# Performance work log

Hardware: AMD Instinct MI355X
Metric: run time of the kernel (lower is better)

## Reference

```python
import jax, jax.numpy as jnp
import numpy as np

# Dimensions (match init_kwargs)
N, B = 32, 16384            # num_elements (agents), batch_size
SD, AD, AD2 = 128, 64, 64   # state_dim, action_dim, action_dim2
IDIM = SD + AD              # per-agent encoder input (obs + act)
H, HEADS = 256, 4           # hidden_dim, attend_heads
AT = H // HEADS             # attend_dim = 64
ODIM = AD                   # critic output = action_dim


def setup_inputs() -> dict:
    key = jax.random.key(0)
    ks = jax.random.split(key, 20)
    g = lambda k, shape: (jax.random.normal(k, shape, jnp.float32) * 0.05)
    return {
        "agent_inputs": jax.random.normal(ks[0], (N, B, IDIM), jnp.float32),
        "state_agent": jax.random.normal(ks[1], (B, SD), jnp.float32),
        "meanfield": jax.random.normal(ks[2], (B, AD), jnp.float32),
        "meanfield2": jax.random.normal(ks[3], (B, AD2), jnp.float32),
        # per-agent critic encoders (enc_fc1)
        "enc_W": g(ks[4], (N, IDIM, H)), "enc_b": g(ks[5], (N, H)),
        # state / meanfield / meanfield2 encoders
        "sW": g(ks[6], (SD, H)), "sb": g(ks[7], (H,)),
        "mfW": g(ks[8], (AD, H)), "mfb": g(ks[9], (H,)),
        "mf2W": g(ks[10], (AD2, H)), "mf2b": g(ks[11], (H,)),
        # per-head key / selector (bias-free) and value extractors
        "Wk": g(ks[12], (HEADS, H, AT)),
        "Wsel": g(ks[13], (HEADS, H, AT)),
        "Wv": g(ks[14], (HEADS, H, AT)), "bv": g(ks[15], (HEADS, AT)),
        # critic head: Linear(4H->H) + LeakyReLU + Linear(H->odim)
        "W1": g(ks[16], (4 * H, H)), "b1": g(ks[17], (H,)),
        "W2": g(ks[18], (H, ODIM)), "b2": g(ks[19], (ODIM,)),
    }


def reference(agent_inputs, state_agent, meanfield, meanfield2,
              enc_W, enc_b, sW, sb, mfW, mfb, mf2W, mf2b,
              Wk, Wsel, Wv, bv, W1, b1, W2, b2):
    lrelu = jax.nn.leaky_relu  # default negative_slope=0.01, matches nn.LeakyReLU
    # Per-agent (obs,act) encoders: [N,B,H]
    sa = lrelu(jnp.einsum('nbi,nih->nbh', agent_inputs, enc_W) + enc_b[:, None, :])
    s_enc = lrelu(state_agent @ sW + sb)          # [B,H]
    mf_enc = lrelu(meanfield @ mfW + mfb)         # [B,H]
    mf2_enc = lrelu(meanfield2 @ mf2W + mf2b)     # [B,H]
    # agents = [0]; keys/values come from all agents except agent 0
    others = sa[1:]                               # [N-1,B,H]
    keys = jnp.einsum('nbh,ehd->enbd', others, Wk)                       # [E,N-1,B,AT]
    vals = lrelu(jnp.einsum('nbh,ehd->enbd', others, Wv) + bv[:, None, None, :])
    sel = jnp.einsum('bh,ehd->ebd', s_enc, Wsel)                         # [E,B,AT]
    logits = jnp.einsum('ebd,enbd->ebn', sel, keys) / jnp.sqrt(jnp.float32(AT))
    w = jax.nn.softmax(logits, axis=-1)                                  # over N-1 agents
    other_vals = jnp.einsum('ebn,enbd->ebd', w, vals)                    # [E,B,AT]
    # concatenate heads in order, matching torch cat over per-head results
    other_flat = jnp.transpose(other_vals, (1, 0, 2)).reshape(B, HEADS * AT)
    critic_in = jnp.concatenate([s_enc, mf_enc, mf2_enc, other_flat], axis=1)  # [B,4H]
    h1 = lrelu(critic_in @ W1 + b1)
    return h1 @ W2 + b2                                                  # all_q: [B,ODIM]
```

## Files before the change

### kernel.cpp

```cpp
#include <hip/hip_runtime.h>
#include <hip/hip_bf16.h>

#define N_AG   32
#define B_SZ   16384
#define SD_    128
#define AD_    64
#define IDIM_  192
#define H_     256
#define HEADS_ 4
#define AT_    64
#define NO_    31

typedef __attribute__((ext_vector_type(8))) short bf16x8_t;
typedef __attribute__((ext_vector_type(4))) float f32x4_t;
typedef __attribute__((ext_vector_type(4))) unsigned int u32x4_t;

__device__ inline unsigned short f2bfu(float f){
  union { __hip_bfloat16 h; unsigned short u; } cv;
  cv.h = __float2bfloat16(f);
  return cv.u;
}
__device__ inline float bflo(unsigned int u){
  union { float f; unsigned int i; } c; c.i = u << 16; return c.f;
}
__device__ inline float bfhi(unsigned int u){
  union { float f; unsigned int i; } c; c.i = u & 0xffff0000u; return c.f;
}

__device__ inline void gll16(const unsigned short* g, unsigned short* l) {
  __builtin_amdgcn_global_load_lds(
      (const __attribute__((address_space(1))) unsigned int*)g,
      (__attribute__((address_space(3))) unsigned int*)l, 16, 0, 0);
}

__device__ inline float dot8(bf16x8_t a, bf16x8_t b, float acc){
  u32x4_t au = __builtin_bit_cast(u32x4_t, a);
  u32x4_t bu = __builtin_bit_cast(u32x4_t, b);
  #pragma unroll
  for (int i = 0; i < 4; i++) {
    acc = fmaf(bflo(au[i]), bflo(bu[i]), acc);
    acc = fmaf(bfhi(au[i]), bfhi(bu[i]), acc);
  }
  return acc;
}

__global__ __launch_bounds__(256) void k_prep(
    const float* __restrict__ encW, const float* __restrict__ sW,
    const float* __restrict__ mfW,  const float* __restrict__ mf2W,
    const float* __restrict__ W1,   const float* __restrict__ W2,
    const float* __restrict__ Wv,   const float* __restrict__ Wsel,
    const float* __restrict__ Wk,
    unsigned short* __restrict__ encWt, unsigned short* __restrict__ sWt,
    unsigned short* __restrict__ mfWt,  unsigned short* __restrict__ mf2Wt,
    unsigned short* __restrict__ W1t,   unsigned short* __restrict__ W2t,
    unsigned short* __restrict__ WvT,   unsigned short* __restrict__ Mct)
{
  const int bid = blockIdx.x, tid = threadIdx.x;
  auto tr = [&](const float* src, unsigned short* dst, int K, int N, int idx){
    int kn = K * N;
    int b = idx / kn, i = idx - b * kn;
    int n = i / K, k = i - n * K;
    dst[(long)b * kn + i] = f2bfu(src[(long)b * kn + (long)k * N + n]);
  };
  if (bid < 5952)        tr(encW + 192*256, encWt, 192, 256, bid*256 + tid);
  else if (bid < 6080)   tr(sW,   sWt,  128, 256, (bid-5952)*256 + tid);
  else if (bid < 6144)   tr(mfW,  mfWt,  64, 256, (bid-6080)*256 + tid);
  else if (bid < 6208)   tr(mf2W, mf2Wt, 64, 256, (bid-6144)*256 + tid);
  else if (bid < 7232)   tr(W1,   W1t, 1024, 256, (bid-6208)*256 + tid);
  else if (bid < 7296)   tr(W2,   W2t,  256,  64, (bid-7232)*256 + tid);
  else if (bid < 7552)   tr(Wv,   WvT,  256,  64, (bid-7296)*256 + tid);
  else {
    int idx = (bid - 7552) * 256 + tid;
    int hp = idx & 255, eh = idx >> 8;
    int e = eh >> 8, h = eh & 255;
    const float* ws = Wsel + ((long)e * 256 + hp) * 64;
    const float* wk = Wk   + ((long)e * 256 + h ) * 64;
    float s = 0.f;
    #pragma unroll 8
    for (int d = 0; d < 64; d++) s += ws[d] * wk[d];
    Mct[idx] = f2bfu(0.125f * s);
  }
}

template<bool AF32, bool LRELU, bool OUTF32>
__global__ __launch_bounds__(512, 2) void k_gemm2(
    const void* __restrict__ Ap, int lda, long strideA,
    const unsigned short* __restrict__ Bt, long strideB,
    const float* __restrict__ bias, long strideBias,
    void* __restrict__ Cp, int ldc, long strideC,
    int K)
{
  __shared__ __align__(16) unsigned short Alds[2][64 * 64];
  __shared__ __align__(16) unsigned short Blds[2][256 * 64];

  const int tid = threadIdx.x;
  const int lane = tid & 63, w = tid >> 6;
  const int wr = w >> 2, wc = w & 3;
  const int lr = lane & 15, lg = lane >> 4;
  const int bm = blockIdx.x, bn = blockIdx.y, bz = blockIdx.z;

  f32x4_t acc[2][4];
  #pragma unroll
  for (int i = 0; i < 2; i++)
    #pragma unroll
    for (int j = 0; j < 4; j++) acc[i][j] = (f32x4_t){0.f, 0.f, 0.f, 0.f};

  const unsigned short* Bb = Bt + bz * strideB + (long)(bn * 256) * K;
  const float* Af32 = AF32 ? (const float*)Ap + bz * strideA + (long)(bm * 64) * lda : nullptr;
  const unsigned short* Abf = AF32 ? nullptr
      : (const unsigned short*)Ap + bz * strideA + (long)(bm * 64) * lda;
  const int nt = K >> 6;

  float4 ar0, ar1;

  auto stageB = [&](int buf, int k0){
    #pragma unroll
    for (int i = 0; i < 4; i++) {
      int c = i * 512 + tid;
      int n = c >> 3, sl = c & 7;
      gll16(Bb + (long)n * K + k0 + (((sl ^ (n & 7)) & 7) << 3), &Blds[buf][c * 8]);
    }
  };
  auto issueA = [&](int buf, int k0){
    if (AF32) {
      int r0 = tid >> 4, q0 = tid & 15;
      ar0 = *reinterpret_cast<const float4*>(Af32 + (long)r0 * lda + k0 + q0 * 4);
      int c1 = tid + 512, r1 = c1 >> 4, q1 = c1 & 15;
      ar1 = *reinterpret_cast<const float4*>(Af32 + (long)r1 * lda + k0 + q1 * 4);
    } else {
      int row = tid >> 3, sl = tid & 7;
      gll16(Abf + (long)row * lda + k0 + (((sl ^ (row & 7)) & 7) << 3),
            &Alds[buf][tid * 8]);
    }
  };
  auto writeA = [&](int buf){
    if (AF32) {
      {
        int c = tid, row = c >> 4, q = c & 15;
        ushort4 u;
        u.x = f2bfu(ar0.x); u.y = f2bfu(ar0.y); u.z = f2bfu(ar0.z); u.w = f2bfu(ar0.w);
        int di = row * 64 + ((((q >> 1) ^ (row & 7)) & 7) << 3) + ((q & 1) << 2);
        *reinterpret_cast<ushort4*>(&Alds[buf][di]) = u;
      }
      {
        int c = tid + 512, row = c >> 4, q = c & 15;
        ushort4 u;
        u.x = f2bfu(ar1.x); u.y = f2bfu(ar1.y); u.z = f2bfu(ar1.z); u.w = f2bfu(ar1.w);
        int di = row * 64 + ((((q >> 1) ^ (row & 7)) & 7) << 3) + ((q & 1) << 2);
        *reinterpret_cast<ushort4*>(&Alds[buf][di]) = u;
      }
    }
  };

  issueA(0, 0);
  stageB(0, 0);
  writeA(0);
  __builtin_amdgcn_sched_barrier(0);
  if (nt > 1) { issueA(1, 64); stageB(1, 64); }
  __builtin_amdgcn_sched_barrier(0);

  for (int t = 0; t < nt; t++) {
    const int cur = t & 1;
    if (t + 1 < nt) {
      if (AF32) asm volatile("s_waitcnt vmcnt(6) lgkmcnt(0)" ::: "memory");
      else      asm volatile("s_waitcnt vmcnt(5) lgkmcnt(0)" ::: "memory");
    } else {
      asm volatile("s_waitcnt vmcnt(0) lgkmcnt(0)" ::: "memory");
    }
    __builtin_amdgcn_s_barrier();
    __builtin_amdgcn_sched_barrier(0);

    bf16x8_t af[2][2], bf[4][2];
    #pragma unroll
    for (int mf = 0; mf < 2; mf++)
      #pragma unroll
      for (int kk = 0; kk < 2; kk++) {
        int row = wr * 32 + mf * 16 + lr;
        af[mf][kk] = *reinterpret_cast<const bf16x8_t*>(
            &Alds[cur][row * 64 + ((((kk * 4 + lg) ^ (row & 7)) & 7) << 3)]);
      }
    #pragma unroll
    for (int nf = 0; nf < 4; nf++)
      #pragma unroll
      for (int kk = 0; kk < 2; kk++) {
        int n = wc * 64 + nf * 16 + lr;
        bf[nf][kk] = *reinterpret_cast<const bf16x8_t*>(
            &Blds[cur][n * 64 + ((((kk * 4 + lg) ^ (n & 7)) & 7) << 3)]);
      }
    #pragma unroll
    for (int kk = 0; kk < 2; kk++)
      #pragma unroll
      for (int mf = 0; mf < 2; mf++)
        #pragma unroll
        for (int nf = 0; nf < 4; nf++)
          acc[mf][nf] = __builtin_amdgcn_mfma_f32_16x16x32_bf16(af[mf][kk], bf[nf][kk], acc[mf][nf], 0, 0, 0);

    __builtin_amdgcn_sched_barrier(0);
    if (t + 1 < nt) writeA(cur ^ 1);
    if (t + 2 < nt) {
      __builtin_amdgcn_s_barrier();
      __builtin_amdgcn_sched_barrier(0);
      issueA(cur, (t + 2) * 64);
      stageB(cur, (t + 2) * 64);
      __builtin_amdgcn_sched_barrier(0);
    }
  }

  const float* bp = bias ? bias + bz * strideBias : nullptr;
  #pragma unroll
  for (int nf = 0; nf < 4; nf++) {
    int col = bn * 256 + wc * 64 + nf * 16 + lr;
    float bvv = bp ? bp[col] : 0.f;
    #pragma unroll
    for (int mf = 0; mf < 2; mf++) {
      #pragma unroll
      for (int r = 0; r < 4; r++) {
        int row = bm * 64 + wr * 32 + mf * 16 + lg * 4 + r;
        float v = acc[mf][nf][r] + bvv;
        if (LRELU) v = v > 0.f ? v : 0.01f * v;
        if (OUTF32)
          ((float*)Cp)[bz * strideC + (long)row * ldc + col] = v;
        else
          ((unsigned short*)Cp)[bz * strideC + (long)row * ldc + col] = f2bfu(v);
      }
    }
  }
}

__global__ __launch_bounds__(512) void k_attnw(
    const unsigned short* __restrict__ others,
    const unsigned short* __restrict__ qbuf,
    float* __restrict__ wbuf,
    float* __restrict__ wsum)
{
  __shared__ __align__(16) unsigned short olds[2][16 * 256];

  const int tid = threadIdx.x;
  const int bm = blockIdx.x;
  const int row = tid >> 5, sub = tid & 31;
  const int e = sub >> 3, ch = sub & 7;
  const long grow = (long)bm * 16 + row;

  bf16x8_t qr[4];
  #pragma unroll
  for (int j = 0; j < 4; j++)
    qr[j] = *reinterpret_cast<const bf16x8_t*>(
        &qbuf[grow * 1024 + e * 256 + ch * 32 + j * 8]);

  float psum = 0.f;

  auto stage = [&](int buf, int n){
    int r = tid >> 5, slot = tid & 31;
    gll16(others + ((long)(bm * 16 + r) * NO_ + n) * 256 + ((slot ^ ((r & 7) << 2)) << 3),
          &olds[buf][tid * 8]);
  };

  stage(0, 0);

  for (int n = 0; n < NO_; n++) {
    const int cur = n & 1;
    __syncthreads();
    if (n + 1 < NO_) stage(cur ^ 1, n + 1);

    float d = 0.f;
    #pragma unroll
    for (int j = 0; j < 4; j++) {
      int slot = (ch * 4 + j) ^ ((row & 7) << 2);
      bf16x8_t o8 = *reinterpret_cast<const bf16x8_t*>(&olds[cur][row * 256 + slot * 8]);
      d = dot8(o8, qr[j], d);
    }
    d += __shfl_xor(d, 1);
    d += __shfl_xor(d, 2);
    d += __shfl_xor(d, 4);
    float p = __expf(d);
    psum += p;
    if (ch == 0) wbuf[grow * 124 + e * 31 + n] = p;
  }
  if (ch == 0) wsum[grow * 4 + e] = psum;
}

__global__ __launch_bounds__(512) void k_pv(
    const unsigned short* __restrict__ others,
    const unsigned short* __restrict__ WvT,
    const float* __restrict__ wbuf,
    const float* __restrict__ wsum,
    const float* __restrict__ bv,
    unsigned short* __restrict__ critic)
{
  __shared__ __align__(16) unsigned short olds[2][16 * 256];
  __shared__ float pl[2][64];

  const int tid = threadIdx.x;
  const int lane = tid & 63, w = tid >> 6;
  const int lr = lane & 15, lg = lane >> 4;
  const int bm = blockIdx.x;
  const int e = w >> 1;

  bf16x8_t wv[2][8];
  #pragma unroll
  for (int nf = 0; nf < 2; nf++)
    #pragma unroll
    for (int kk = 0; kk < 8; kk++)
      wv[nf][kk] = *reinterpret_cast<const bf16x8_t*>(
          &WvT[(long)(w * 32 + nf * 16 + lr) * 256 + kk * 32 + lg * 8]);
  float bvv[2] = { bv[w * 32 + lr], bv[w * 32 + 16 + lr] };

  f32x4_t outa[2];
  outa[0] = (f32x4_t){0.f, 0.f, 0.f, 0.f};
  outa[1] = (f32x4_t){0.f, 0.f, 0.f, 0.f};

  auto stage = [&](int buf, int n){
    int r = tid >> 5, slot = tid & 31;
    gll16(others + ((long)(bm * 16 + r) * NO_ + n) * 256 + ((slot ^ ((r & 7) << 2)) << 3),
          &olds[buf][tid * 8]);
  };
  auto stagep = [&](int buf, int n){
    if (tid < 64)
      pl[buf][tid] = wbuf[((long)bm * 16 + (tid >> 2)) * 124 + (tid & 3) * 31 + n];
  };

  stage(0, 0); stagep(0, 0);

  for (int n = 0; n < NO_; n++) {
    const int cur = n & 1;
    __syncthreads();
    if (n + 1 < NO_) { stage(cur ^ 1, n + 1); stagep(cur ^ 1, n + 1); }

    f32x4_t va[2];
    va[0] = (f32x4_t){0.f, 0.f, 0.f, 0.f};
    va[1] = (f32x4_t){0.f, 0.f, 0.f, 0.f};
    #pragma unroll
    for (int kk = 0; kk < 8; kk++) {
      bf16x8_t af = *reinterpret_cast<const bf16x8_t*>(
          &olds[cur][lr * 256 + (((kk * 4 + lg) ^ ((lr & 7) << 2)) << 3)]);
      va[0] = __builtin_amdgcn_mfma_f32_16x16x32_bf16(af, wv[0][kk], va[0], 0, 0, 0);
      va[1] = __builtin_amdgcn_mfma_f32_16x16x32_bf16(af, wv[1][kk], va[1], 0, 0, 0);
    }

    #pragma unroll
    for (int r = 0; r < 4; r++) {
      float p = pl[cur][(lg * 4 + r) * 4 + e];
      #pragma unroll
      for (int nf = 0; nf < 2; nf++) {
        float v = va[nf][r] + bvv[nf];
        v = v > 0.f ? v : 0.01f * v;
        outa[nf][r] += p * v;
      }
    }
  }

  #pragma unroll
  for (int r = 0; r < 4; r++) {
    long grow = (long)bm * 16 + lg * 4 + r;
    float inv = 1.f / wsum[grow * 4 + e];
    #pragma unroll
    for (int nf = 0; nf < 2; nf++)
      critic[grow * 1024 + 768 + w * 32 + nf * 16 + lr] = f2bfu(outa[nf][r] * inv);
  }
}

template<bool AF32, bool LRELU, bool OUTF32>
__global__ __launch_bounds__(256) void k_gemm(
    const void* __restrict__ Ap, int lda, long strideA,
    const unsigned short* __restrict__ Bt, long strideB,
    const float* __restrict__ bias, long strideBias,
    void* __restrict__ Cp, int ldc, long strideC,
    int K)
{
  __shared__ __align__(16) unsigned short Alds[128][40];
  __shared__ __align__(16) unsigned short Blds[64][40];

  const int tid = threadIdx.x;
  const int bm = blockIdx.x, bn = blockIdx.y, bz = blockIdx.z;
  const int w = tid >> 6, lane = tid & 63;
  const int wr = (w >> 1) * 64, wc = (w & 1) * 32;
  const int lr = lane & 15, lk = (lane >> 4) * 8;

  f32x4_t acc[4][2];
  #pragma unroll
  for (int i = 0; i < 4; i++)
    #pragma unroll
    for (int j = 0; j < 2; j++) acc[i][j] = (f32x4_t){0.f, 0.f, 0.f, 0.f};

  const unsigned short* Bb = Bt + bz * strideB + (long)(bn * 64) * K;

  for (int k0 = 0; k0 < K; k0 += 32) {
    if (AF32) {
      const float* A = (const float*)Ap + bz * strideA + (long)(bm * 128) * lda + k0;
      #pragma unroll
      for (int i = 0; i < 4; i++) {
        int chunk = tid + i * 256;
        int m = chunk >> 3, kc = (chunk & 7) * 4;
        const float4 v = *reinterpret_cast<const float4*>(A + (long)m * lda + kc);
        ushort4 p;
        p.x = f2bfu(v.x); p.y = f2bfu(v.y); p.z = f2bfu(v.z); p.w = f2bfu(v.w);
        *reinterpret_cast<ushort4*>(&Alds[m][kc]) = p;
      }
    } else {
      const unsigned short* A = (const unsigned short*)Ap + bz * strideA + (long)(bm * 128) * lda + k0;
      #pragma unroll
      for (int i = 0; i < 4; i++) {
        int chunk = tid + i * 256;
        int m = chunk >> 3, kc = (chunk & 7) * 4;
        *reinterpret_cast<ushort4*>(&Alds[m][kc]) =
            *reinterpret_cast<const ushort4*>(A + (long)m * lda + kc);
      }
    }
    #pragma unroll
    for (int i = 0; i < 2; i++) {
      int chunk = tid + i * 256;
      int n = chunk >> 3, kc = (chunk & 7) * 4;
      *reinterpret_cast<ushort4*>(&Blds[n][kc]) =
          *reinterpret_cast<const ushort4*>(Bb + (long)n * K + k0 + kc);
    }
    __syncthreads();

    bf16x8_t bfr0 = *reinterpret_cast<const bf16x8_t*>(&Blds[wc + lr][lk]);
    bf16x8_t bfr1 = *reinterpret_cast<const bf16x8_t*>(&Blds[wc + 16 + lr][lk]);
    #pragma unroll
    for (int mf = 0; mf < 4; mf++) {
      bf16x8_t afr = *reinterpret_cast<const bf16x8_t*>(&Alds[wr + mf * 16 + lr][lk]);
      acc[mf][0] = __builtin_amdgcn_mfma_f32_16x16x32_bf16(afr, bfr0, acc[mf][0], 0, 0, 0);
      acc[mf][1] = __builtin_amdgcn_mfma_f32_16x16x32_bf16(afr, bfr1, acc[mf][1], 0, 0, 0);
    }
    __syncthreads();
  }

  const float* bp = bias ? bias + bz * strideBias : nullptr;
  #pragma unroll
  for (int nf = 0; nf < 2; nf++) {
    int col = bn * 64 + wc + nf * 16 + lr;
    float bvv = bp ? bp[col] : 0.f;
    #pragma unroll
    for (int mf = 0; mf < 4; mf++) {
      #pragma unroll
      for (int r = 0; r < 4; r++) {
        int row = bm * 128 + wr + mf * 16 + (lane >> 4) * 4 + r;
        float v = acc[mf][nf][r] + bvv;
        if (LRELU) v = v > 0.f ? v : 0.01f * v;
        if (OUTF32)
          ((float*)Cp)[bz * strideC + (long)row * ldc + col] = v;
        else
          ((unsigned short*)Cp)[bz * strideC + (long)row * ldc + col] = f2bfu(v);
      }
    }
  }
}

extern "C" void kernel_launch(void* const* d_in, const int* in_sizes, int n_in,
                              void* d_out, int out_size, void* d_ws, size_t ws_size,
                              hipStream_t stream)
{
  (void)in_sizes; (void)n_in; (void)out_size; (void)ws_size;
  const float* agent = (const float*)d_in[0];
  const float* state = (const float*)d_in[1];
  const float* mf    = (const float*)d_in[2];
  const float* mf2   = (const float*)d_in[3];
  const float* encW  = (const float*)d_in[4];
  const float* encb  = (const float*)d_in[5];
  const float* sW    = (const float*)d_in[6];
  const float* sb    = (const float*)d_in[7];
  const float* mfW   = (const float*)d_in[8];
  const float* mfb   = (const float*)d_in[9];
  const float* mf2W  = (const float*)d_in[10];
  const float* mf2b  = (const float*)d_in[11];
  const float* Wk    = (const float*)d_in[12];
  const float* Wsel  = (const float*)d_in[13];
  const float* Wv    = (const float*)d_in[14];
  const float* bv    = (const float*)d_in[15];
  const float* W1    = (const float*)d_in[16];
  const float* b1    = (const float*)d_in[17];
  const float* W2    = (const float*)d_in[18];
  const float* b2    = (const float*)d_in[19];
  float* out = (float*)d_out;

  char* ws = (char*)d_ws;
  size_t off = 0;
  auto alloc = [&](size_t bytes) -> char* {
    char* p = ws + off; off += (bytes + 255) & ~(size_t)255; return p;
  };
  unsigned short* others = (unsigned short*)alloc((size_t)B_SZ * NO_ * H_ * 2);
  unsigned short* qbuf   = (unsigned short*)alloc((size_t)B_SZ * 1024 * 2);
  unsigned short* critic = (unsigned short*)alloc((size_t)B_SZ * 1024 * 2);
  unsigned short* h1buf  = (unsigned short*)alloc((size_t)B_SZ * H_ * 2);
  float*          wbuf   = (float*)alloc((size_t)B_SZ * HEADS_ * NO_ * 4);
  float*          wsum   = (float*)alloc((size_t)B_SZ * HEADS_ * 4);
  unsigned short* encWt  = (unsigned short*)alloc((size_t)NO_ * H_ * IDIM_ * 2);
  unsigned short* Mct    = (unsigned short*)alloc((size_t)1024 * 256 * 2);
  unsigned short* WvT    = (unsigned short*)alloc((size_t)256 * 256 * 2);
  unsigned short* sWt    = (unsigned short*)alloc((size_t)256 * 128 * 2);
  unsigned short* mfWt   = (unsigned short*)alloc((size_t)256 * 64 * 2);
  unsigned short* mf2Wt  = (unsigned short*)alloc((size_t)256 * 64 * 2);
  unsigned short* W1t    = (unsigned short*)alloc((size_t)256 * 1024 * 2);
  unsigned short* W2t    = (unsigned short*)alloc((size_t)64 * 256 * 2);

  k_prep<<<dim3(8576), 256, 0, stream>>>(
      encW, sW, mfW, mf2W, W1, W2, Wv, Wsel, Wk,
      encWt, sWt, mfWt, mf2Wt, W1t, W2t, WvT, Mct);

  k_gemm2<true, true, false><<<dim3(256, 1, NO_), 512, 0, stream>>>(
      agent + (size_t)B_SZ * IDIM_, IDIM_, (long)B_SZ * IDIM_,
      encWt, (long)H_ * IDIM_,
      encb + H_, H_,
      others, NO_ * H_, H_, IDIM_);

  k_gemm2<true, true, false><<<dim3(256, 1, 1), 512, 0, stream>>>(
      state, SD_, 0, sWt, 0, sb, 0, critic, 1024, 0, SD_);
  k_gemm2<true, true, false><<<dim3(256, 1, 1), 512, 0, stream>>>(
      mf, AD_, 0, mfWt, 0, mfb, 0, critic + 256, 1024, 0, AD_);
  k_gemm2<true, true, false><<<dim3(256, 1, 1), 512, 0, stream>>>(
      mf2, AD_, 0, mf2Wt, 0, mf2b, 0, critic + 512, 1024, 0, AD_);

  k_gemm2<false, false, false><<<dim3(256, 4, 1), 512, 0, stream>>>(
      critic, 1024, 0, Mct, 0, nullptr, 0, qbuf, 1024, 0, 256);

  k_attnw<<<dim3(B_SZ / 16), 512, 0, stream>>>(others, qbuf, wbuf, wsum);

  k_pv<<<dim3(B_SZ / 16), 512, 0, stream>>>(others, WvT, wbuf, wsum, bv, critic);

  k_gemm2<false, true, false><<<dim3(256, 1, 1), 512, 0, stream>>>(
      critic, 1024, 0, W1t, 0, b1, 0, h1buf, H_, 0, 1024);

  k_gemm<false, false, true><<<dim3(128, 1, 1), 256, 0, stream>>>(
      h1buf, H_, 0, W2t, 0, b2, 0, out, 64, 0, 256);
}
```

Before: 446.1 us.

## Fuse attention-weight and value kernels into one LDS-resident pass

Merges the logits/softmax kernel and the value-projection kernel into one kernel. Each block loads all 31 agent encodings for 8 batch rows into LDS once, computes the exp weights into shared memory, then runs the MFMA value projection and weighted sum from the same LDS copy. This removes the second global read of the large others tensor and the wbuf/wsum round trip. In exchange it uses about 127 KB of LDS per block, which limits occupancy and drops the double-buffered overlap of loads and compute.

```diff
diff --git a/kernel.cpp b/kernel.cpp
--- a/kernel.cpp
+++ b/kernel.cpp
@@ -227,74 +227,39 @@
   }
 }
 
-__global__ __launch_bounds__(512) void k_attnw(
+__global__ __launch_bounds__(512) void k_attnpv(
     const unsigned short* __restrict__ others,
     const unsigned short* __restrict__ qbuf,
-    float* __restrict__ wbuf,
-    float* __restrict__ wsum)
-{
-  __shared__ __align__(16) unsigned short olds[2][16 * 256];
-
-  const int tid = threadIdx.x;
-  const int bm = blockIdx.x;
-  const int row = tid >> 5, sub = tid & 31;
-  const int e = sub >> 3, ch = sub & 7;
-  const long grow = (long)bm * 16 + row;
-
-  bf16x8_t qr[4];
-  #pragma unroll
-  for (int j = 0; j < 4; j++)
-    qr[j] = *reinterpret_cast<const bf16x8_t*>(
-        &qbuf[grow * 1024 + e * 256 + ch * 32 + j * 8]);
-
-  float psum = 0.f;
-
-  auto stage = [&](int buf, int n){
-    int r = tid >> 5, slot = tid & 31;
-    gll16(others + ((long)(bm * 16 + r) * NO_ + n) * 256 + ((slot ^ ((r & 7) << 2)) << 3),
-          &olds[buf][tid * 8]);
-  };
-
-  stage(0, 0);
-
-  for (int n = 0; n < NO_; n++) {
-    const int cur = n & 1;
-    __syncthreads();
-    if (n + 1 < NO_) stage(cur ^ 1, n + 1);
-
-    float d = 0.f;
-    #pragma unroll
-    for (int j = 0; j < 4; j++) {
-      int slot = (ch * 4 + j) ^ ((row & 7) << 2);
-      bf16x8_t o8 = *reinterpret_cast<const bf16x8_t*>(&olds[cur][row * 256 + slot * 8]);
-      d = dot8(o8, qr[j], d);
-    }
-    d += __shfl_xor(d, 1);
-    d += __shfl_xor(d, 2);
-    d += __shfl_xor(d, 4);
-    float p = __expf(d);
-    psum += p;
-    if (ch == 0) wbuf[grow * 124 + e * 31 + n] = p;
-  }
-  if (ch == 0) wsum[grow * 4 + e] = psum;
-}
-
-__global__ __launch_bounds__(512) void k_pv(
-    const unsigned short* __restrict__ others,
     const unsigned short* __restrict__ WvT,
-    const float* __restrict__ wbuf,
-    const float* __restrict__ wsum,
     const float* __restrict__ bv,
     unsigned short* __restrict__ critic)
 {
-  __shared__ __align__(16) unsigned short olds[2][16 * 256];
-  __shared__ float pl[2][64];
+  __shared__ __align__(16) unsigned short oth[8 * 31 * 256];
+  __shared__ float pbuf[8][4][32];
+  __shared__ float psbuf[8][4];
 
   const int tid = threadIdx.x;
   const int lane = tid & 63, w = tid >> 6;
   const int lr = lane & 15, lg = lane >> 4;
   const int bm = blockIdx.x;
-  const int e = w >> 1;
+
+  #pragma unroll
+  for (int i = 0; i < 16; i++) {
+    int c = i * 512 + tid;
+    if (c < 7936) {
+      int row31 = c >> 5, slot = c & 31;
+      int r = row31 / 31, n = row31 - r * 31;
+      gll16(others + ((long)(bm * 8 + r) * NO_ + n) * 256 + ((slot ^ ((row31 & 7) << 2)) << 3),
+            &oth[c * 8]);
+    }
+  }
+
+  const int qrow = w, qe = lg, qch = lr;
+  bf16x8_t qr[2];
+  qr[0] = *reinterpret_cast<const bf16x8_t*>(
+      &qbuf[((long)(bm * 8 + qrow)) * 1024 + qe * 256 + qch * 16]);
+  qr[1] = *reinterpret_cast<const bf16x8_t*>(
+      &qbuf[((long)(bm * 8 + qrow)) * 1024 + qe * 256 + qch * 16 + 8]);
 
   bf16x8_t wv[2][8];
   #pragma unroll
@@ -305,26 +270,46 @@
           &WvT[(long)(w * 32 + nf * 16 + lr) * 256 + kk * 32 + lg * 8]);
   float bvv[2] = { bv[w * 32 + lr], bv[w * 32 + 16 + lr] };
 
+  __syncthreads();
+
+  {
+    float psum = 0.f;
+    const int rbase = qrow * NO_;
+    for (int n = 0; n < NO_; n++) {
+      int row31 = rbase + n;
+      int sw = (row31 & 7) << 2;
+      bf16x8_t o0 = *reinterpret_cast<const bf16x8_t*>(
+          &oth[row31 * 256 + (((qch * 2) ^ sw) << 3)]);
+      bf16x8_t o1 = *reinterpret_cast<const bf16x8_t*>(
+          &oth[row31 * 256 + (((qch * 2 + 1) ^ sw) << 3)]);
+      float d = dot8(o0, qr[0], 0.f);
+      d = dot8(o1, qr[1], d);
+      d += __shfl_xor(d, 1);
+      d += __shfl_xor(d, 2);
+      d += __shfl_xor(d, 4);
+      d += __shfl_xor(d, 8);
+      float p = __expf(d);
+      if (qch == 0) { psum += p; pbuf[qrow][qe][n] = p; }
+    }
+    if (qch == 0) psbuf[qrow][qe] = psum;
+  }
+
+  __syncthreads();
+
+  const int e = w >> 1;
   f32x4_t outa[2];
   outa[0] = (f32x4_t){0.f, 0.f, 0.f, 0.f};
   outa[1] = (f32x4_t){0.f, 0.f, 0.f, 0.f};
 
-  auto stage = [&](int buf, int n){
-    int r = tid >> 5, slot = tid & 31;
-    gll16(others + ((long)(bm * 16 + r) * NO_ + n) * 256 + ((slot ^ ((r & 7) << 2)) << 3),
-          &olds[buf][tid * 8]);
-  };
-  auto stagep = [&](int buf, int n){
-    if (tid < 64)
-      pl[buf][tid] = wbuf[((long)bm * 16 + (tid >> 2)) * 124 + (tid & 3) * 31 + n];
-  };
-
-  stage(0, 0); stagep(0, 0);
-
-  for (int n = 0; n < NO_; n++) {
-    const int cur = n & 1;
-    __syncthreads();
-    if (n + 1 < NO_) { stage(cur ^ 1, n + 1); stagep(cur ^ 1, n + 1); }
+  const int nhA = lr >> 3;
+  const int nhC = lg >> 1;
+  const int browC = (lg & 1) * 4;
+
+  for (int np = 0; np < 16; np++) {
+    int nnA = np * 2 + nhA;
+    int nnAc = nnA > 30 ? 30 : nnA;
+    int row31 = (lr & 7) * NO_ + nnAc;
+    int sw = (row31 & 7) << 2;
 
     f32x4_t va[2];
     va[0] = (f32x4_t){0.f, 0.f, 0.f, 0.f};
@@ -332,14 +317,15 @@
     #pragma unroll
     for (int kk = 0; kk < 8; kk++) {
       bf16x8_t af = *reinterpret_cast<const bf16x8_t*>(
-          &olds[cur][lr * 256 + (((kk * 4 + lg) ^ ((lr & 7) << 2)) << 3)]);
+          &oth[row31 * 256 + (((kk * 4 + lg) ^ sw) << 3)]);
       va[0] = __builtin_amdgcn_mfma_f32_16x16x32_bf16(af, wv[0][kk], va[0], 0, 0, 0);
       va[1] = __builtin_amdgcn_mfma_f32_16x16x32_bf16(af, wv[1][kk], va[1], 0, 0, 0);
     }
 
+    int n2 = np * 2 + nhC;
     #pragma unroll
     for (int r = 0; r < 4; r++) {
-      float p = pl[cur][(lg * 4 + r) * 4 + e];
+      float p = (n2 < NO_) ? pbuf[browC + r][e][n2] : 0.f;
       #pragma unroll
       for (int nf = 0; nf < 2; nf++) {
         float v = va[nf][r] + bvv[nf];
@@ -350,12 +336,21 @@
   }
 
   #pragma unroll
-  for (int r = 0; r < 4; r++) {
-    long grow = (long)bm * 16 + lg * 4 + r;
-    float inv = 1.f / wsum[grow * 4 + e];
-    #pragma unroll
-    for (int nf = 0; nf < 2; nf++)
-      critic[grow * 1024 + 768 + w * 32 + nf * 16 + lr] = f2bfu(outa[nf][r] * inv);
+  for (int nf = 0; nf < 2; nf++)
+    #pragma unroll
+    for (int r = 0; r < 4; r++)
+      outa[nf][r] += __shfl_xor(outa[nf][r], 32);
+
+  if (lg < 2) {
+    #pragma unroll
+    for (int r = 0; r < 4; r++) {
+      int brow = browC + r;
+      long grow = (long)bm * 8 + brow;
+      float inv = 1.f / psbuf[brow][e];
+      #pragma unroll
+      for (int nf = 0; nf < 2; nf++)
+        critic[grow * 1024 + 768 + w * 32 + nf * 16 + lr] = f2bfu(outa[nf][r] * inv);
+    }
   }
 }
 
@@ -483,8 +478,6 @@
   unsigned short* qbuf   = (unsigned short*)alloc((size_t)B_SZ * 1024 * 2);
   unsigned short* critic = (unsigned short*)alloc((size_t)B_SZ * 1024 * 2);
   unsigned short* h1buf  = (unsigned short*)alloc((size_t)B_SZ * H_ * 2);
-  float*          wbuf   = (float*)alloc((size_t)B_SZ * HEADS_ * NO_ * 4);
-  float*          wsum   = (float*)alloc((size_t)B_SZ * HEADS_ * 4);
   unsigned short* encWt  = (unsigned short*)alloc((size_t)NO_ * H_ * IDIM_ * 2);
   unsigned short* Mct    = (unsigned short*)alloc((size_t)1024 * 256 * 2);
   unsigned short* WvT    = (unsigned short*)alloc((size_t)256 * 256 * 2);
@@ -514,9 +507,7 @@
   k_gemm2<false, false, false><<<dim3(256, 4, 1), 512, 0, stream>>>(
       critic, 1024, 0, Mct, 0, nullptr, 0, qbuf, 1024, 0, 256);
 
-  k_attnw<<<dim3(B_SZ / 16), 512, 0, stream>>>(others, qbuf, wbuf, wsum);
-
-  k_pv<<<dim3(B_SZ / 16), 512, 0, stream>>>(others, WvT, wbuf, wsum, bv, critic);
+  k_attnpv<<<dim3(B_SZ / 8), 512, 0, stream>>>(others, qbuf, WvT, bv, critic);
 
   k_gemm2<false, true, false><<<dim3(256, 1, 1), 512, 0, stream>>>(
       critic, 1024, 0, W1t, 0, b1, 0, h1buf, H_, 0, 1024);
```

After: 474.8 us. 1.06x slower.
